# Kernel tuning notes

Hardware: AMD Instinct MI355X
Metric: run time of the kernel (lower is better)

The kernel has to match this reference:

```python
import jax, jax.numpy as jnp
import numpy as np

B, C, H, W = 4, 64, 128, 128
Q = 65536
OUT_SIZE = 256  # output image side -> cell = 2/OUT_SIZE
HIDDEN = 256
D_IN = C + 2 + 2  # feat + rel_coord + rel_cell


def setup_inputs() -> dict:
    key = jax.random.key(0)
    ks = jax.random.split(key, 8)
    feat = jax.random.normal(ks[0], (B, C, H, W), dtype=jnp.float32)
    coord = jax.random.uniform(ks[1], (B, Q, 2), dtype=jnp.float32, minval=-1.0, maxval=1.0)
    cell = jnp.full((B, Q, 2), 2.0 / OUT_SIZE, dtype=jnp.float32)

    def lin(k, din, dout):
        return jax.random.normal(k, (din, dout), dtype=jnp.float32) * (1.0 / np.sqrt(din))

    w0 = lin(ks[2], D_IN, HIDDEN)
    w1 = lin(ks[3], HIDDEN, HIDDEN)
    w2 = lin(ks[4], HIDDEN, HIDDEN)
    w3 = lin(ks[5], HIDDEN, HIDDEN)
    w4 = lin(ks[6], HIDDEN, 3)
    z = lambda d: jnp.zeros((d,), dtype=jnp.float32)
    return {"feat": feat, "coord": coord, "cell": cell,
            "w0": w0, "b0": z(HIDDEN), "w1": w1, "b1": z(HIDDEN),
            "w2": w2, "b2": z(HIDDEN), "w3": w3, "b3": z(HIDDEN),
            "w4": w4, "b4": z(3)}


def _liif(feat, coord, cell, ws, bs):
    b, c, h, w = feat.shape
    eps = 1e-6
    rx, ry = 1.0 / h, 1.0 / w  # 2/h/2, 2/w/2
    # local ensemble shifts, loop order vx outer, vy inner: (-1,-1),(-1,1),(1,-1),(1,1)
    shifts = jnp.array([[-rx, -ry], [-rx, ry], [rx, -ry], [rx, ry]], dtype=feat.dtype) + eps
    feat_flat = feat.reshape(b, c, h * w)
    cell_scale = jnp.array([h, w], dtype=feat.dtype)
    rel_cell = cell * cell_scale  # same for all branches

    def branch(shift):
        cshift = jnp.clip(coord + shift, -1.0 + eps, 1.0 - eps)
        # nearest grid_sample, align_corners=False: idx = floor((x+1)*size/2), clamped
        iy = jnp.clip(jnp.floor((cshift[..., 0] + 1.0) * (h * 0.5)), 0.0, h - 1.0).astype(jnp.int32)
        ix = jnp.clip(jnp.floor((cshift[..., 1] + 1.0) * (w * 0.5)), 0.0, w - 1.0).astype(jnp.int32)
        idx = iy * w + ix  # [B, Q]
        q_feat = jnp.take_along_axis(feat_flat, idx[:, None, :], axis=2)  # [B, C, Q]
        q_feat = q_feat.transpose(0, 2, 1)  # [B, Q, C]
        # feat_coord at the gathered pixel (make_coord values)
        qc0 = -1.0 + (2.0 * iy.astype(feat.dtype) + 1.0) / h
        qc1 = -1.0 + (2.0 * ix.astype(feat.dtype) + 1.0) / w
        rel0 = (coord[..., 0] - qc0) * h
        rel1 = (coord[..., 1] - qc1) * w
        inp = jnp.concatenate([q_feat, rel0[..., None], rel1[..., None], rel_cell], axis=-1)
        x = inp
        for wi, bi in zip(ws[:-1], bs[:-1]):
            x = jax.nn.relu(x @ wi + bi)
        pred = x @ ws[-1] + bs[-1]  # [B, Q, 3]
        area = jnp.abs(rel0 * rel1) + 1e-9  # [B, Q]
        return pred, area

    preds, areas = jax.vmap(branch)(shifts)  # [4,B,Q,3], [4,B,Q]
    tot = areas.sum(axis=0)
    # diagonal weight swap: 0<->3, 1<->2  == reverse
    wgt = areas[::-1] / tot
    return (preds * wgt[..., None]).sum(axis=0)  # [B, Q, 3]


def reference(feat, coord, cell, w0, b0, w1, b1, w2, b2, w3, b3, w4, b4):
    ws = [w0, w1, w2, w3, w4]
    bs = [b0, b1, b2, b3, b4]
    return _liif(feat, coord, cell, ws, bs)
```

## Files before the change

### kernel.cpp

```cpp
#include <hip/hip_runtime.h>
#include <cstdint>

typedef __bf16 bf16x8 __attribute__((ext_vector_type(8)));
typedef float f32x4 __attribute__((ext_vector_type(4)));
typedef float f32x16 __attribute__((ext_vector_type(16)));
typedef unsigned int u32x4 __attribute__((ext_vector_type(4)));
typedef unsigned int u32x2 __attribute__((ext_vector_type(2)));
typedef unsigned short u16;
typedef unsigned int u32;

#define HH 128
#define WW 128
#define CC 64
#define QQ 65536
#define BB 4

#define RS 264

#define L0_OFF 0
#define L1_OFF 20480
#define L2_OFF 86016
#define L3_OFF 151552
#define W4_OFF 217088
#define FEATT_BYTE_OFF 524288u

__global__ void pack_weights(const float* __restrict__ w0,
                             const float* __restrict__ w1,
                             const float* __restrict__ w2,
                             const float* __restrict__ w3,
                             const float* __restrict__ w4,
                             u16* __restrict__ ws_us) {
    int bid = blockIdx.x;
    int lane = threadIdx.x;
    int dst, kbase, n, Ksrc, Ncols;
    const float* w;
    if (bid < 424) {
        int tile, off;
        if (bid < 40)       { tile = bid;       off = L0_OFF; w = w0; Ksrc = 68;  }
        else if (bid < 168) { tile = bid - 40;  off = L1_OFF; w = w1; Ksrc = 256; }
        else if (bid < 296) { tile = bid - 168; off = L2_OFF; w = w2; Ksrc = 256; }
        else                { tile = bid - 296; off = L3_OFF; w = w3; Ksrc = 256; }
        int nt = tile & 7, ks = tile >> 3;
        n = nt * 32 + (lane & 31);
        kbase = ks * 16 + (lane >> 5) * 8;
        Ncols = 256;
        dst = off + tile * 512 + lane * 8;
    } else {
        int kt = bid - 424;
        n = lane & 15;
        kbase = kt * 32 + (lane >> 4) * 8;
        w = w4; Ksrc = 256; Ncols = 3;
        dst = W4_OFF + kt * 512 + lane * 8;
    }
    unsigned int d[4];
    for (int i = 0; i < 4; ++i) {
        unsigned int lo, hi;
        {
            int k = kbase + 2 * i;
            float x = (k < Ksrc && n < Ncols) ? w[k * Ncols + n] : 0.0f;
            __bf16 hb = (__bf16)x;
            lo = (unsigned int)__builtin_bit_cast(u16, hb);
        }
        {
            int k = kbase + 2 * i + 1;
            float x = (k < Ksrc && n < Ncols) ? w[k * Ncols + n] : 0.0f;
            __bf16 hb = (__bf16)x;
            hi = (unsigned int)__builtin_bit_cast(u16, hb);
        }
        d[i] = lo | (hi << 16);
    }
    u32x4 pk = { d[0], d[1], d[2], d[3] };
    *reinterpret_cast<u32x4*>(ws_us + dst) = pk;
}

__global__ void prep_featT(const float* __restrict__ feat, u16* __restrict__ featT) {
    __shared__ u16 tile[128 * 66];
    int bid = blockIdx.x;
    int b = bid >> 7, y = bid & 127;
    for (int idx = threadIdx.x; idx < CC * WW; idx += 256) {
        int c = idx >> 7, x = idx & 127;
        float v = feat[(((b * CC + c) * HH + y) * WW) + x];
        __bf16 hb = (__bf16)v;
        tile[x * 66 + c] = __builtin_bit_cast(u16, hb);
    }
    __syncthreads();
    for (int idx = threadIdx.x; idx < 2048; idx += 256) {
        int x = idx >> 4, c4 = (idx & 15) * 4;
        const u16* src = tile + x * 66 + c4;
        u32x2 d;
        d[0] = (unsigned int)src[0] | ((unsigned int)src[1] << 16);
        d[1] = (unsigned int)src[2] | ((unsigned int)src[3] << 16);
        *reinterpret_cast<u32x2*>(featT + ((b * HH + y) * WW + x) * CC + c4) = d;
    }
}

__device__ __forceinline__ void preload32(u32x4 w[4], const u32x4* __restrict__ b,
                                          int v) {
    w[0] = b[v];
    w[1] = b[v + 64];
    w[2] = b[v + 512];
    w[3] = b[v + 576];
}

template <int NKS>
__device__ __forceinline__ void gemm32(u16* buf,
                                       const u32x4* __restrict__ wbase,
                                       const float* __restrict__ bias,
                                       int wave, int lane,
                                       const u32x4 wpre[4],
                                       u32x4 wnxt[4],
                                       const u32x4* __restrict__ wnb,
                                       int vnxt, int nstride2) {
    f32x16 acc[2][2] = {};
    const int l31 = lane & 31;
    const int hi = lane >> 5;
    const int voff = wave * 128 + lane;
    const u16* xb = buf + l31 * RS + hi * 8;
    u16* db = buf + l31 * RS + wave * 64 + hi * 4;

    u32x4 wq[2][2];
    wq[0][0] = wpre[0]; wq[0][1] = wpre[1];
    wq[1][0] = wpre[2]; wq[1][1] = wpre[3];

    bf16x8 xc[2];
    xc[0] = __builtin_bit_cast(bf16x8, *reinterpret_cast<const u32x4*>(xb));
    xc[1] = __builtin_bit_cast(bf16x8, *reinterpret_cast<const u32x4*>(xb + 32 * RS));

#pragma unroll
    for (int ks = 0; ks < NKS; ++ks) {
        acc[0][0] = __builtin_amdgcn_mfma_f32_32x32x16_bf16(
            __builtin_bit_cast(bf16x8, wq[ks & 1][0]), xc[0], acc[0][0], 0, 0, 0);
        acc[1][0] = __builtin_amdgcn_mfma_f32_32x32x16_bf16(
            __builtin_bit_cast(bf16x8, wq[ks & 1][1]), xc[0], acc[1][0], 0, 0, 0);
        if (ks + 1 < NKS)
            xc[0] = __builtin_bit_cast(bf16x8,
                *reinterpret_cast<const u32x4*>(xb + (ks + 1) * 16));
        acc[0][1] = __builtin_amdgcn_mfma_f32_32x32x16_bf16(
            __builtin_bit_cast(bf16x8, wq[ks & 1][0]), xc[1], acc[0][1], 0, 0, 0);
        acc[1][1] = __builtin_amdgcn_mfma_f32_32x32x16_bf16(
            __builtin_bit_cast(bf16x8, wq[ks & 1][1]), xc[1], acc[1][1], 0, 0, 0);
        if (ks + 1 < NKS)
            xc[1] = __builtin_bit_cast(bf16x8,
                *reinterpret_cast<const u32x4*>(xb + 32 * RS + (ks + 1) * 16));
        if (ks + 2 < NKS) {
            const u32x4* wn = wbase + (ks + 2) * 512;
            wq[ks & 1][0] = wn[voff];
            wq[ks & 1][1] = wn[voff + 64];
        }
    }

    wnxt[0] = wnb[vnxt];
    wnxt[1] = wnb[vnxt + 64];
    wnxt[2] = wnb[vnxt + nstride2];
    wnxt[3] = wnb[vnxt + nstride2 + 64];

    __syncthreads();

#pragma unroll
    for (int ft = 0; ft < 2; ++ft) {
        const int fb = wave * 64 + ft * 32 + hi * 4;
#pragma unroll
        for (int q4 = 0; q4 < 4; ++q4) {
            f32x4 bv = *reinterpret_cast<const f32x4*>(bias + fb + q4 * 8);
#pragma unroll
            for (int st = 0; st < 2; ++st) {
                float v0 = fmaxf(acc[ft][st][q4 * 4 + 0] + bv[0], 0.0f);
                float v1 = fmaxf(acc[ft][st][q4 * 4 + 1] + bv[1], 0.0f);
                float v2 = fmaxf(acc[ft][st][q4 * 4 + 2] + bv[2], 0.0f);
                float v3 = fmaxf(acc[ft][st][q4 * 4 + 3] + bv[3], 0.0f);
                __bf16 h0 = (__bf16)v0, h1 = (__bf16)v1, h2 = (__bf16)v2, h3 = (__bf16)v3;
                u32x2 d;
                d[0] = (u32)__builtin_bit_cast(u16, h0) | ((u32)__builtin_bit_cast(u16, h1) << 16);
                d[1] = (u32)__builtin_bit_cast(u16, h2) | ((u32)__builtin_bit_cast(u16, h3) << 16);
                *reinterpret_cast<u32x2*>(db + st * 32 * RS + ft * 32 + q4 * 8) = d;
            }
        }
    }
}

__global__ __launch_bounds__(256, 4) void liif_main(
    const float* __restrict__ coord, const float* __restrict__ cell,
    const float* __restrict__ b0, const float* __restrict__ b1,
    const float* __restrict__ b2, const float* __restrict__ b3,
    const float* __restrict__ b4,
    const u16* __restrict__ wpack, const u16* __restrict__ featT,
    float* __restrict__ out) {
    __shared__ u16 bufA[64 * RS];
    __shared__ float areasLDS[64];

    const int t = threadIdx.x;
    const int wave = t >> 6, lane = t & 63;
    const int row = t >> 2, p = t & 3;

    const int bq = blockIdx.x * 16 + (row >> 2);
    const int v = row & 3;
    const int b = bq >> 16;
    const float c0 = coord[bq * 2 + 0];
    const float c1 = coord[bq * 2 + 1];
    const float rc0 = cell[bq * 2 + 0] * 128.0f;
    const float rc1 = cell[bq * 2 + 1] * 128.0f;
    const float eps = 1e-6f;
    const float sx = ((v & 2) ? 0.0078125f : -0.0078125f) + eps;
    const float sy = ((v & 1) ? 0.0078125f : -0.0078125f) + eps;
    float cs0 = fminf(fmaxf(c0 + sx, -1.0f + eps), 1.0f - eps);
    float cs1 = fminf(fmaxf(c1 + sy, -1.0f + eps), 1.0f - eps);
    float fy = fminf(fmaxf(floorf((cs0 + 1.0f) * 64.0f), 0.0f), 127.0f);
    float fx = fminf(fmaxf(floorf((cs1 + 1.0f) * 64.0f), 0.0f), 127.0f);
    int iy = (int)fy, ix = (int)fx;
    float qc0 = -1.0f + (2.0f * fy + 1.0f) * 0.0078125f;
    float qc1 = -1.0f + (2.0f * fx + 1.0f) * 0.0078125f;
    float rel0 = (c0 - qc0) * 128.0f;
    float rel1 = (c1 - qc1) * 128.0f;
    float area = fabsf(rel0 * rel1) + 1e-9f;

    {
        const u16* fr = featT + (((b * HH + iy) * WW + ix) * CC) + p * 16;
        u32x4 f0 = *reinterpret_cast<const u32x4*>(fr);
        u32x4 f1 = *reinterpret_cast<const u32x4*>(fr + 8);
        u16* sb = bufA + row * RS;
        *reinterpret_cast<u32x4*>(sb + p * 16) = f0;
        *reinterpret_cast<u32x4*>(sb + p * 16 + 8) = f1;
        u32x4 e = { 0u, 0u, 0u, 0u };
        if (p == 0) {
            __bf16 h0 = (__bf16)rel0, h1 = (__bf16)rel1, h2 = (__bf16)rc0, h3 = (__bf16)rc1;
            e[0] = (u32)__builtin_bit_cast(u16, h0) | ((u32)__builtin_bit_cast(u16, h1) << 16);
            e[1] = (u32)__builtin_bit_cast(u16, h2) | ((u32)__builtin_bit_cast(u16, h3) << 16);
            areasLDS[row] = area;
        }
        *reinterpret_cast<u32x4*>(sb + 64 + p * 8) = e;
    }

    const u32x4* wp = reinterpret_cast<const u32x4*>(wpack);
    const u32x4* wp0 = wp + (L0_OFF / 8);
    const u32x4* wp1 = wp + (L1_OFF / 8);
    const u32x4* wp2 = wp + (L2_OFF / 8);
    const u32x4* wp3 = wp + (L3_OFF / 8);
    const u32x4* wp4 = wp + (W4_OFF / 8);
    const int voff = wave * 128 + lane;

    u32x4 wA[4], wB[4];
    preload32(wA, wp0, voff);
    __syncthreads();
    gemm32<5>(bufA, wp0, b0, wave, lane, wA, wB, wp1, voff, 512);
    __syncthreads();
    gemm32<16>(bufA, wp1, b1, wave, lane, wB, wA, wp2, voff, 512);
    __syncthreads();
    gemm32<16>(bufA, wp2, b2, wave, lane, wA, wB, wp3, voff, 512);
    __syncthreads();
    gemm32<16>(bufA, wp3, b3, wave, lane, wB, wA, wp4, lane, 128);
    u32x4 w4hi[4];
#pragma unroll
    for (int kt = 0; kt < 4; ++kt) w4hi[kt] = wp4[(kt + 4) * 64 + lane];
    __syncthreads();

    const int l15 = lane & 15;
    const int qd = lane >> 4;
    const u16* xb = bufA + (wave * 16 + l15) * RS + qd * 8;
    f32x4 accf = {};
#pragma unroll
    for (int kt = 0; kt < 4; ++kt) {
        bf16x8 x = __builtin_bit_cast(bf16x8,
            *reinterpret_cast<const u32x4*>(xb + kt * 32));
        accf = __builtin_amdgcn_mfma_f32_16x16x32_bf16(
            __builtin_bit_cast(bf16x8, wA[kt]), x, accf, 0, 0, 0);
    }
#pragma unroll
    for (int kt = 4; kt < 8; ++kt) {
        bf16x8 x = __builtin_bit_cast(bf16x8,
            *reinterpret_cast<const u32x4*>(xb + kt * 32));
        accf = __builtin_amdgcn_mfma_f32_16x16x32_bf16(
            __builtin_bit_cast(bf16x8, w4hi[kt - 4]), x, accf, 0, 0, 0);
    }
    float a = areasLDS[wave * 16 + l15];
    float a1 = a + __shfl_xor(a, 1);
    float asum = a1 + __shfl_xor(a1, 2);
    float aopp = __shfl_xor(a, 3);
    float wgt = aopp / asum;
    float o0 = (accf[0] + b4[0]) * wgt;
    float o1 = (accf[1] + b4[1]) * wgt;
    float o2 = (accf[2] + b4[2]) * wgt;
    o0 += __shfl_xor(o0, 1); o0 += __shfl_xor(o0, 2);
    o1 += __shfl_xor(o1, 1); o1 += __shfl_xor(o1, 2);
    o2 += __shfl_xor(o2, 1); o2 += __shfl_xor(o2, 2);

    if (qd == 0 && (l15 & 3) == 0) {
        int obq = blockIdx.x * 16 + wave * 4 + (l15 >> 2);
        out[obq * 3 + 0] = o0;
        out[obq * 3 + 1] = o1;
        out[obq * 3 + 2] = o2;
    }
}

extern "C" void kernel_launch(void* const* d_in, const int* in_sizes, int n_in,
                              void* d_out, int out_size, void* d_ws, size_t ws_size,
                              hipStream_t stream) {
    const float* feat  = (const float*)d_in[0];
    const float* coord = (const float*)d_in[1];
    const float* cell  = (const float*)d_in[2];
    const float* w0 = (const float*)d_in[3];
    const float* b0 = (const float*)d_in[4];
    const float* w1 = (const float*)d_in[5];
    const float* b1 = (const float*)d_in[6];
    const float* w2 = (const float*)d_in[7];
    const float* b2 = (const float*)d_in[8];
    const float* w3 = (const float*)d_in[9];
    const float* b3 = (const float*)d_in[10];
    const float* w4 = (const float*)d_in[11];
    const float* b4 = (const float*)d_in[12];

    u16* ws_us = (u16*)d_ws;
    u16* featT = (u16*)((char*)d_ws + FEATT_BYTE_OFF);

    hipLaunchKernelGGL(pack_weights, dim3(432), dim3(64), 0, stream,
                       w0, w1, w2, w3, w4, ws_us);
    hipLaunchKernelGGL(prep_featT, dim3(BB * HH), dim3(256), 0, stream, feat, featT);
    hipLaunchKernelGGL(liif_main, dim3((BB * QQ) / 16), dim3(256), 0, stream,
                       coord, cell, b0, b1, b2, b3, b4, ws_us, featT,
                       (float*)d_out);
}
```

Measured before the change: 550.3 us.

## Ping-pong LDS activation buffers and deepen weight/activation prefetch in MLP GEMMs

Each MLP layer now reads activations from one LDS buffer and writes to another, which removes the barrier between the K-loop and the epilogue write. Weight prefetch goes from two to three stages and activation fragments are loaded two k-steps ahead, to hide more global and LDS latency. The cost is double the LDS and more registers, so launch bounds drop from 4 to 2 blocks per CU, which lowers occupancy. The final layer preload is adjusted to the 6-register weight arrays.

```diff
diff --git a/kernel.cpp b/kernel.cpp
--- a/kernel.cpp
+++ b/kernel.cpp
@@ -94,67 +94,75 @@
     }
 }
 
-__device__ __forceinline__ void preload32(u32x4 w[4], const u32x4* __restrict__ b,
-                                          int v) {
+__device__ __forceinline__ void preload6(u32x4 w[6], const u32x4* __restrict__ b,
+                                         int v, int kstr) {
     w[0] = b[v];
     w[1] = b[v + 64];
-    w[2] = b[v + 512];
-    w[3] = b[v + 576];
+    w[2] = b[v + kstr];
+    w[3] = b[v + kstr + 64];
+    w[4] = b[v + 2 * kstr];
+    w[5] = b[v + 2 * kstr + 64];
 }
 
 template <int NKS>
-__device__ __forceinline__ void gemm32(u16* buf,
+__device__ __forceinline__ void gemm32(const u16* __restrict__ src,
+                                       u16* __restrict__ dst,
                                        const u32x4* __restrict__ wbase,
                                        const float* __restrict__ bias,
                                        int wave, int lane,
-                                       const u32x4 wpre[4],
-                                       u32x4 wnxt[4],
+                                       const u32x4 wpre[6],
+                                       u32x4 wnxt[6],
                                        const u32x4* __restrict__ wnb,
-                                       int vnxt, int nstride2) {
+                                       int vnxt, int nkstr) {
     f32x16 acc[2][2] = {};
     const int l31 = lane & 31;
     const int hi = lane >> 5;
     const int voff = wave * 128 + lane;
-    const u16* xb = buf + l31 * RS + hi * 8;
-    u16* db = buf + l31 * RS + wave * 64 + hi * 4;
-
-    u32x4 wq[2][2];
+    const u16* xb = src + l31 * RS + hi * 8;
+    u16* db = dst + l31 * RS + wave * 64 + hi * 4;
+
+    u32x4 wq[3][2];
     wq[0][0] = wpre[0]; wq[0][1] = wpre[1];
     wq[1][0] = wpre[2]; wq[1][1] = wpre[3];
-
-    bf16x8 xc[2];
-    xc[0] = __builtin_bit_cast(bf16x8, *reinterpret_cast<const u32x4*>(xb));
-    xc[1] = __builtin_bit_cast(bf16x8, *reinterpret_cast<const u32x4*>(xb + 32 * RS));
+    wq[2][0] = wpre[4]; wq[2][1] = wpre[5];
+
+    bf16x8 xc[2][2];
+    xc[0][0] = __builtin_bit_cast(bf16x8, *reinterpret_cast<const u32x4*>(xb));
+    xc[0][1] = __builtin_bit_cast(bf16x8, *reinterpret_cast<const u32x4*>(xb + 32 * RS));
+    xc[1][0] = __builtin_bit_cast(bf16x8, *reinterpret_cast<const u32x4*>(xb + 16));
+    xc[1][1] = __builtin_bit_cast(bf16x8, *reinterpret_cast<const u32x4*>(xb + 32 * RS + 16));
 
 #pragma unroll
     for (int ks = 0; ks < NKS; ++ks) {
+        const int ws = ks % 3;
+        const int xs = ks & 1;
         acc[0][0] = __builtin_amdgcn_mfma_f32_32x32x16_bf16(
-            __builtin_bit_cast(bf16x8, wq[ks & 1][0]), xc[0], acc[0][0], 0, 0, 0);
+            __builtin_bit_cast(bf16x8, wq[ws][0]), xc[xs][0], acc[0][0], 0, 0, 0);
         acc[1][0] = __builtin_amdgcn_mfma_f32_32x32x16_bf16(
-            __builtin_bit_cast(bf16x8, wq[ks & 1][1]), xc[0], acc[1][0], 0, 0, 0);
-        if (ks + 1 < NKS)
-            xc[0] = __builtin_bit_cast(bf16x8,
-                *reinterpret_cast<const u32x4*>(xb + (ks + 1) * 16));
+            __builtin_bit_cast(bf16x8, wq[ws][1]), xc[xs][0], acc[1][0], 0, 0, 0);
+        if (ks + 2 < NKS)
+            xc[xs][0] = __builtin_bit_cast(bf16x8,
+                *reinterpret_cast<const u32x4*>(xb + (ks + 2) * 16));
         acc[0][1] = __builtin_amdgcn_mfma_f32_32x32x16_bf16(
-            __builtin_bit_cast(bf16x8, wq[ks & 1][0]), xc[1], acc[0][1], 0, 0, 0);
+            __builtin_bit_cast(bf16x8, wq[ws][0]), xc[xs][1], acc[0][1], 0, 0, 0);
         acc[1][1] = __builtin_amdgcn_mfma_f32_32x32x16_bf16(
-            __builtin_bit_cast(bf16x8, wq[ks & 1][1]), xc[1], acc[1][1], 0, 0, 0);
-        if (ks + 1 < NKS)
-            xc[1] = __builtin_bit_cast(bf16x8,
-                *reinterpret_cast<const u32x4*>(xb + 32 * RS + (ks + 1) * 16));
-        if (ks + 2 < NKS) {
-            const u32x4* wn = wbase + (ks + 2) * 512;
-            wq[ks & 1][0] = wn[voff];
-            wq[ks & 1][1] = wn[voff + 64];
+            __builtin_bit_cast(bf16x8, wq[ws][1]), xc[xs][1], acc[1][1], 0, 0, 0);
+        if (ks + 2 < NKS)
+            xc[xs][1] = __builtin_bit_cast(bf16x8,
+                *reinterpret_cast<const u32x4*>(xb + 32 * RS + (ks + 2) * 16));
+        if (ks + 3 < NKS) {
+            const u32x4* wn = wbase + (ks + 3) * 512;
+            wq[ws][0] = wn[voff];
+            wq[ws][1] = wn[voff + 64];
         }
     }
 
     wnxt[0] = wnb[vnxt];
     wnxt[1] = wnb[vnxt + 64];
-    wnxt[2] = wnb[vnxt + nstride2];
-    wnxt[3] = wnb[vnxt + nstride2 + 64];
-
-    __syncthreads();
+    wnxt[2] = wnb[vnxt + nkstr];
+    wnxt[3] = wnb[vnxt + nkstr + 64];
+    wnxt[4] = wnb[vnxt + 2 * nkstr];
+    wnxt[5] = wnb[vnxt + 2 * nkstr + 64];
 
 #pragma unroll
     for (int ft = 0; ft < 2; ++ft) {
@@ -178,15 +186,18 @@
     }
 }
 
-__global__ __launch_bounds__(256, 4) void liif_main(
+__global__ __launch_bounds__(256, 2) void liif_main(
     const float* __restrict__ coord, const float* __restrict__ cell,
     const float* __restrict__ b0, const float* __restrict__ b1,
     const float* __restrict__ b2, const float* __restrict__ b3,
     const float* __restrict__ b4,
     const u16* __restrict__ wpack, const u16* __restrict__ featT,
     float* __restrict__ out) {
-    __shared__ u16 bufA[64 * RS];
+    __shared__ u16 bufs[2 * 64 * RS];
     __shared__ float areasLDS[64];
+
+    u16* buf0 = bufs;
+    u16* buf1 = bufs + 64 * RS;
 
     const int t = threadIdx.x;
     const int wave = t >> 6, lane = t & 63;
@@ -217,7 +228,7 @@
         const u16* fr = featT + (((b * HH + iy) * WW + ix) * CC) + p * 16;
         u32x4 f0 = *reinterpret_cast<const u32x4*>(fr);
         u32x4 f1 = *reinterpret_cast<const u32x4*>(fr + 8);
-        u16* sb = bufA + row * RS;
+        u16* sb = buf0 + row * RS;
         *reinterpret_cast<u32x4*>(sb + p * 16) = f0;
         *reinterpret_cast<u32x4*>(sb + p * 16 + 8) = f1;
         u32x4 e = { 0u, 0u, 0u, 0u };
@@ -238,38 +249,38 @@
     const u32x4* wp4 = wp + (W4_OFF / 8);
     const int voff = wave * 128 + lane;
 
-    u32x4 wA[4], wB[4];
-    preload32(wA, wp0, voff);
-    __syncthreads();
-    gemm32<5>(bufA, wp0, b0, wave, lane, wA, wB, wp1, voff, 512);
-    __syncthreads();
-    gemm32<16>(bufA, wp1, b1, wave, lane, wB, wA, wp2, voff, 512);
-    __syncthreads();
-    gemm32<16>(bufA, wp2, b2, wave, lane, wA, wB, wp3, voff, 512);
-    __syncthreads();
-    gemm32<16>(bufA, wp3, b3, wave, lane, wB, wA, wp4, lane, 128);
-    u32x4 w4hi[4];
-#pragma unroll
-    for (int kt = 0; kt < 4; ++kt) w4hi[kt] = wp4[(kt + 4) * 64 + lane];
+    u32x4 wA[6], wB[6];
+    preload6(wA, wp0, voff, 512);
+    __syncthreads();
+    gemm32<5>(buf0, buf1, wp0, b0, wave, lane, wA, wB, wp1, voff, 512);
+    __syncthreads();
+    gemm32<16>(buf1, buf0, wp1, b1, wave, lane, wB, wA, wp2, voff, 512);
+    __syncthreads();
+    gemm32<16>(buf0, buf1, wp2, b2, wave, lane, wA, wB, wp3, voff, 512);
+    __syncthreads();
+    gemm32<16>(buf1, buf0, wp3, b3, wave, lane, wB, wA, wp4, lane, 128);
+    u32x4 w4hi[2];
+#pragma unroll
+    for (int kt = 0; kt < 2; ++kt) w4hi[kt] = wp4[(kt + 6) * 64 + lane];
     __syncthreads();
 
     const int l15 = lane & 15;
     const int qd = lane >> 4;
-    const u16* xb = bufA + (wave * 16 + l15) * RS + qd * 8;
+    const u16* xb = buf0 + (wave * 16 + l15) * RS + qd * 8;
     f32x4 accf = {};
 #pragma unroll
-    for (int kt = 0; kt < 4; ++kt) {
+    for (int kt = 0; kt < 6; ++kt) {
         bf16x8 x = __builtin_bit_cast(bf16x8,
             *reinterpret_cast<const u32x4*>(xb + kt * 32));
         accf = __builtin_amdgcn_mfma_f32_16x16x32_bf16(
             __builtin_bit_cast(bf16x8, wA[kt]), x, accf, 0, 0, 0);
     }
 #pragma unroll
-    for (int kt = 4; kt < 8; ++kt) {
+    for (int kt = 6; kt < 8; ++kt) {
         bf16x8 x = __builtin_bit_cast(bf16x8,
             *reinterpret_cast<const u32x4*>(xb + kt * 32));
         accf = __builtin_amdgcn_mfma_f32_16x16x32_bf16(
-            __builtin_bit_cast(bf16x8, w4hi[kt - 4]), x, accf, 0, 0, 0);
+            __builtin_bit_cast(bf16x8, w4hi[kt - 6]), x, accf, 0, 0, 0);
     }
     float a = areasLDS[wave * 16 + l15];
     float a1 = a + __shfl_xor(a, 1);
```

Result: slower. 579.0 us (+5.2%).
